# Performance work log

Hardware: AMD Instinct MI355X
Metric: run time of the kernel (lower is better)

Reference implementation:

```python
import jax, jax.numpy as jnp
import numpy as np

DELTA_VAR = 0.5
DELTA_DIST = 1.5
ALPHA, BETA, GAMMA = 1.0, 1.0, 0.001
EPS = 1e-8


def _safe_sqrt(x):
    # sqrt with zero (sub)gradient at 0, matching torch.norm's subgradient
    pos = x > 0
    return jnp.sqrt(jnp.where(pos, x, 1.0)) * pos


def setup_inputs() -> dict:
    key = jax.random.key(0)
    k1, k2, k3 = jax.random.split(key, 3)
    B, F, H, W, K = 8, 16, 384, 384, 24
    x = jax.random.normal(k1, (B, F, H, W), dtype=jnp.float32)
    n_clusters = jax.random.randint(k2, (B,), 2, K + 1).astype(jnp.int32)
    # per-pixel instance labels, in-range per sample
    labels = jax.random.randint(k3, (B, H * W), 0, K) % n_clusters[:, None]
    target = jax.nn.one_hot(labels, K, dtype=jnp.float32)  # (B, L, K)
    target = target.transpose(0, 2, 1).reshape(B, K, H, W)
    return {"input": x, "target": target, "n_clusters": n_clusters}


def reference(input, target, n_clusters):
    B, F, H, W = input.shape
    K = target.shape[1]
    x = input.reshape(B, F, H * W)          # (b, f, l)
    t = target.reshape(B, K, H * W)         # (b, c, l)
    nc = n_clusters.astype(x.dtype)         # (b,)
    valid = (jnp.arange(K)[None, :] < n_clusters[:, None]).astype(x.dtype)  # (b, c)

    # ---- cluster means (masked segment mean; padded clusters -> 0) ----
    t_sum = t.sum(-1)                                        # (b, c)
    sums = jnp.einsum('bfl,bcl->bfc', x, t)                  # (b, f, c)
    means = sums / (t_sum[:, None, :] + EPS) * valid[:, None, :]

    # ---- variance term: ||x_l - mu_c||_2 via quadratic expansion ----
    x2 = jnp.sum(x * x, axis=1)                              # (b, l)
    m2 = jnp.sum(means * means, axis=1)                      # (b, c)
    xm = jnp.einsum('bfl,bfc->bcl', x, means)                # (b, c, l)
    d2 = jnp.maximum(x2[:, None, :] - 2.0 * xm + m2[:, :, None], 0.0)
    dist = _safe_sqrt(d2)                                    # (b, c, l)
    var = jnp.maximum(dist - DELTA_VAR, 0.0) ** 2 * t        # (b, c, l)
    c_var = var.sum(-1) / (t_sum + EPS)                      # (b, c)
    var_per = (c_var * valid).sum(-1) / (nc + EPS)
    var_term = jnp.sum(var_per * (nc > 0)) / B

    # ---- distance term: hinge on pairwise mean distances ----
    mm = jnp.einsum('bfc,bfd->bcd', means, means)            # (b, c, c)
    pd2 = jnp.maximum(m2[:, :, None] - 2.0 * mm + m2[:, None, :], 0.0)
    pdist = _safe_sqrt(pd2)                                  # (b, c, c)
    offdiag = 1.0 - jnp.eye(K, dtype=x.dtype)
    pair_mask = valid[:, :, None] * valid[:, None, :] * offdiag
    hinge = jnp.maximum(2.0 * DELTA_DIST - pdist, 0.0) ** 2 * pair_mask
    dist_per = hinge.sum((1, 2)) / (2.0 * nc * (nc - 1.0) + EPS)
    dist_term = jnp.sum(dist_per * (nc > 1)) / B

    # ---- regularization term: mean over valid clusters of ||mu_c|| ----
    norms = _safe_sqrt(m2)                                   # (b, c)
    reg_term = jnp.sum((norms * valid).sum(-1) / nc) / B

    return ALPHA * var_term + BETA * dist_term + GAMMA * reg_term
```

## Files before the change

### kernel.cpp

```cpp
#include <hip/hip_runtime.h>

#define B 8
#define F 16
#define K 24
#define L 147456
#define CHUNK1 1024
#define NCH1 144
#define TOTCH 1152
#define EPSF 1e-8f
#define DELTA_VAR 0.5f
#define DELTA_DIST 1.5f
#define GAMMA 0.001f

typedef float fx4 __attribute__((ext_vector_type(4)));
typedef short bf16x8 __attribute__((ext_vector_type(8)));
typedef float f32x4 __attribute__((ext_vector_type(4)));

#define OFF_CNTP 1769472
#define OFF_VARP 1880064
#define OFF_CNT  1990656
#define OFF_MEAN 1991424
#define OFF_LAB  2003968

__device__ __forceinline__ short to_bf16(float v) {
    unsigned u = __float_as_uint(v);
    return (short)((u + 0x7FFFu + ((u >> 16) & 1u)) >> 16);
}

__global__ __launch_bounds__(256, 3) void k1_sums(
        const float* __restrict__ t, const float* __restrict__ x,
        unsigned char* __restrict__ labels, float* __restrict__ cnt_part,
        float* __restrict__ sum_part) {
    const int gblk = blockIdx.x;
    const int b = gblk / NCH1;
    const int ch = gblk % NCH1;
    const int tid = threadIdx.x;
    const int wave = tid >> 6;
    const int lane = tid & 63;
    const int n = lane & 15;
    const int q = lane >> 4;

    __shared__ unsigned char slab[CHUNK1];
    __shared__ float hist[4][32];
    __shared__ float sacc[4][F * K];

    if (lane < 32) hist[wave][lane] = 0.f;

    const float* xr = x + (size_t)(b * F + n) * L + ch * CHUNK1 + wave * 256 + q * 8;
    fx4 xv[16];
    #pragma unroll
    for (int it = 0; it < 8; ++it) {
        xv[2 * it]     = *(const fx4*)(xr + it * 32);
        xv[2 * it + 1] = *(const fx4*)(xr + it * 32 + 4);
    }
    __builtin_amdgcn_sched_barrier(0);

    const int px = ch * CHUNK1 + tid * 4;
    const fx4* t4 = (const fx4*)t;
    int lab0 = 0, lab1 = 0, lab2 = 0, lab3 = 0;
    #pragma unroll
    for (int h = 0; h < 3; ++h) {
        fx4 tv[8];
        #pragma unroll
        for (int j = 0; j < 8; ++j)
            tv[j] = __builtin_nontemporal_load(
                &t4[((size_t)(b * K + h * 8 + j) * L + px) >> 2]);
        __builtin_amdgcn_sched_barrier(0);
        #pragma unroll
        for (int j = 0; j < 8; ++j) {
            int c = h * 8 + j;
            lab0 += c * (tv[j].x > 0.5f);
            lab1 += c * (tv[j].y > 0.5f);
            lab2 += c * (tv[j].z > 0.5f);
            lab3 += c * (tv[j].w > 0.5f);
        }
    }
    uchar4 lv = make_uchar4((unsigned char)lab0, (unsigned char)lab1,
                            (unsigned char)lab2, (unsigned char)lab3);
    *(uchar4*)&labels[(size_t)b * L + px] = lv;
    *(uchar4*)&slab[tid * 4] = lv;
    atomicAdd(&hist[wave][lab0], 1.f);
    atomicAdd(&hist[wave][lab1], 1.f);
    atomicAdd(&hist[wave][lab2], 1.f);
    atomicAdd(&hist[wave][lab3], 1.f);
    __syncthreads();
    if (tid < K) {
        float v = hist[0][tid] + hist[1][tid] + hist[2][tid] + hist[3][tid];
        cnt_part[tid * TOTCH + gblk] = v;
    }

    const unsigned char* sl = slab + wave * 256 + q * 8;
    f32x4 acc0 = {0.f, 0.f, 0.f, 0.f};
    f32x4 acc1 = {0.f, 0.f, 0.f, 0.f};
    #pragma unroll
    for (int it = 0; it < 8; ++it) {
        unsigned l0 = *(const unsigned*)(sl + it * 32);
        unsigned l1 = *(const unsigned*)(sl + it * 32 + 4);
        fx4 xa = xv[2 * it], xc = xv[2 * it + 1];

        bf16x8 afrag;
        afrag[0] = to_bf16(xa.x); afrag[1] = to_bf16(xa.y);
        afrag[2] = to_bf16(xa.z); afrag[3] = to_bf16(xa.w);
        afrag[4] = to_bf16(xc.x); afrag[5] = to_bf16(xc.y);
        afrag[6] = to_bf16(xc.z); afrag[7] = to_bf16(xc.w);

        bf16x8 bf0, bf1;
        #pragma unroll
        for (int j = 0; j < 8; ++j) {
            int lj = (j < 4) ? ((l0 >> (8 * j)) & 0xFF) : ((l1 >> (8 * (j - 4))) & 0xFF);
            bf0[j] = (lj == n)      ? (short)0x3F80 : (short)0;
            bf1[j] = (lj == n + 16) ? (short)0x3F80 : (short)0;
        }
        acc0 = __builtin_amdgcn_mfma_f32_16x16x32_bf16(afrag, bf0, acc0, 0, 0, 0);
        acc1 = __builtin_amdgcn_mfma_f32_16x16x32_bf16(afrag, bf1, acc1, 0, 0, 0);
    }

    #pragma unroll
    for (int r = 0; r < 4; ++r) {
        int f = q * 4 + r;
        sacc[wave][f * K + n] = acc0[r];
        if (n < 8) sacc[wave][f * K + 16 + n] = acc1[r];
    }
    __syncthreads();
    for (int i = tid; i < F * K; i += 256) {
        float v = sacc[0][i] + sacc[1][i] + sacc[2][i] + sacc[3][i];
        sum_part[(size_t)i * TOTCH + gblk] = v;
    }
}

__global__ __launch_bounds__(256) void k2_means(const float* __restrict__ cnt_part,
                                                const float* __restrict__ sum_part,
                                                const int* __restrict__ ncl,
                                                float* __restrict__ counts,
                                                float* __restrict__ means) {
    const int idx = blockIdx.x * 4 + (threadIdx.x >> 6);
    const int lane = threadIdx.x & 63;
    const int b = idx / (F * K);
    const int r = idx % (F * K);
    const int c = r % K;

    const float* crow = cnt_part + c * TOTCH + b * NCH1;
    const float* srow = sum_part + (size_t)r * TOTCH + b * NCH1;
    float cv = crow[lane] + crow[lane + 64] + ((lane < 16) ? crow[lane + 128] : 0.f);
    float sv = srow[lane] + srow[lane + 64] + ((lane < 16) ? srow[lane + 128] : 0.f);
    #pragma unroll
    for (int off = 32; off > 0; off >>= 1) {
        cv += __shfl_down(cv, off);
        sv += __shfl_down(sv, off);
    }
    if (lane == 0) {
        if (r < K) counts[b * K + c] = cv;
        float valid = (c < ncl[b]) ? 1.f : 0.f;
        means[b * F * K + r] = sv / (cv + EPSF) * valid;
    }
}

__global__ __launch_bounds__(256, 4) void k3_var(
        const float* __restrict__ x, const unsigned char* __restrict__ labels,
        const float* __restrict__ means, float* __restrict__ var_part) {
    const int gblk = blockIdx.x;
    const int b = gblk / NCH1;
    const int ch = gblk % NCH1;
    const int tid = threadIdx.x;
    const int wave = tid >> 6;
    const int lane = tid & 63;

    __shared__ float m[F * K];
    __shared__ float hist[4][32];

    const int px = ch * CHUNK1 + tid * 4;
    uchar4 lv = *(const uchar4*)&labels[(size_t)b * L + px];
    const fx4* x4 = (const fx4*)x;
    fx4 xv[F];
    #pragma unroll
    for (int f = 0; f < F; ++f)
        xv[f] = x4[((size_t)(b * F + f) * L + px) >> 2];
    __builtin_amdgcn_sched_barrier(0);

    for (int i = tid; i < F * K; i += 256) m[i] = means[b * F * K + i];
    if (lane < 32) hist[wave][lane] = 0.f;
    __syncthreads();

    float d0 = 0.f, d1 = 0.f, d2 = 0.f, d3 = 0.f;
    #pragma unroll
    for (int f = 0; f < F; ++f) {
        float u0 = xv[f].x - m[f * K + lv.x]; d0 += u0 * u0;
        float u1 = xv[f].y - m[f * K + lv.y]; d1 += u1 * u1;
        float u2 = xv[f].z - m[f * K + lv.z]; d2 += u2 * u2;
        float u3 = xv[f].w - m[f * K + lv.w]; d3 += u3 * u3;
    }
    float s0 = fmaxf(sqrtf(d0) - DELTA_VAR, 0.f); s0 *= s0;
    float s1 = fmaxf(sqrtf(d1) - DELTA_VAR, 0.f); s1 *= s1;
    float s2 = fmaxf(sqrtf(d2) - DELTA_VAR, 0.f); s2 *= s2;
    float s3 = fmaxf(sqrtf(d3) - DELTA_VAR, 0.f); s3 *= s3;
    atomicAdd(&hist[wave][lv.x], s0);
    atomicAdd(&hist[wave][lv.y], s1);
    atomicAdd(&hist[wave][lv.z], s2);
    atomicAdd(&hist[wave][lv.w], s3);
    __syncthreads();
    if (tid < K) {
        float v = hist[0][tid] + hist[1][tid] + hist[2][tid] + hist[3][tid];
        var_part[tid * TOTCH + gblk] = v;
    }
}

__global__ __launch_bounds__(256) void k4_finish(
        const float* __restrict__ var_part, const float* __restrict__ means,
        const float* __restrict__ counts, const int* __restrict__ ncl,
        float* __restrict__ out) {
    __shared__ float big[B * F * K];
    __shared__ float vs[192], cn[192], red[256];
    const int tid = threadIdx.x;

    for (int i = tid; i < B * F * K; i += 256) big[i] = means[i];
    if (tid < 192) {
        int bb = tid / K, c = tid % K;
        const float* row = var_part + c * TOTCH + bb * NCH1;
        float s = 0.f;
        #pragma unroll 8
        for (int j = 0; j < NCH1; ++j) s += row[j];
        vs[tid] = s;
        cn[tid] = counts[tid];
    }
    __syncthreads();

    float total = 0.f;
    for (int idx = tid; idx < B * K * K; idx += 256) {
        int bb = idx / (K * K);
        int r = idx % (K * K);
        int c = r / K;
        int d = r % K;
        int ncb = ncl[bb];
        float fnc = (float)ncb;
        if (d == 0 && c < ncb && ncb > 0) {
            float cv = vs[bb * K + c] / (cn[bb * K + c] + EPSF);
            total += cv / (fnc + EPSF) * (1.0f / B);
            float m2 = 0.f;
            #pragma unroll
            for (int f = 0; f < F; ++f) {
                float mv = big[(bb * F + f) * K + c];
                m2 += mv * mv;
            }
            total += GAMMA * sqrtf(m2) / fnc * (1.0f / B);
        }
        if (c != d && c < ncb && d < ncb && ncb > 1) {
            float pd2 = 0.f;
            #pragma unroll
            for (int f = 0; f < F; ++f) {
                float diff = big[(bb * F + f) * K + c] - big[(bb * F + f) * K + d];
                pd2 += diff * diff;
            }
            float h = fmaxf(2.f * DELTA_DIST - sqrtf(pd2), 0.f);
            total += h * h / (2.f * fnc * (fnc - 1.f) + EPSF) * (1.0f / B);
        }
    }
    red[tid] = total;
    __syncthreads();
    for (int s = 128; s > 0; s >>= 1) {
        if (tid < s) red[tid] += red[tid + s];
        __syncthreads();
    }
    if (tid == 0) out[0] = red[0];
}

extern "C" void kernel_launch(void* const* d_in, const int* in_sizes, int n_in,
                              void* d_out, int out_size, void* d_ws, size_t ws_size,
                              hipStream_t stream) {
    const float* x = (const float*)d_in[0];
    const float* t = (const float*)d_in[1];
    const int* ncl = (const int*)d_in[2];
    float* out = (float*)d_out;

    char* ws = (char*)d_ws;
    float* sum_part = (float*)ws;
    float* cnt_part = (float*)(ws + OFF_CNTP);
    float* var_part = (float*)(ws + OFF_VARP);
    float* counts   = (float*)(ws + OFF_CNT);
    float* means    = (float*)(ws + OFF_MEAN);
    unsigned char* labels = (unsigned char*)(ws + OFF_LAB);

    k1_sums <<<TOTCH, 256, 0, stream>>>(t, x, labels, cnt_part, sum_part);
    k2_means<<<768, 256, 0, stream>>>(cnt_part, sum_part, ncl, counts, means);
    k3_var  <<<TOTCH, 256, 0, stream>>>(x, labels, means, var_part);
    k4_finish<<<1, 256, 0, stream>>>(var_part, means, counts, ncl, out);
}
```

Before: 243.6 us.

## Interleave batches across blocks, transpose sum partials, parallelize variance reduction

Blocks are remapped so consecutive block IDs cycle over batches instead of walking chunks within one batch. The k1 partial-sum layout becomes chunk-major so its writes are contiguous, and k2 reads are strided to match. The serial per-thread variance reduction in the single-block finish kernel moves into a new 48-block wave-shuffle reduction kernel. The extra launch adds a little overhead, and k2 now reads strided instead of contiguous.

```diff
diff --git a/kernel.cpp b/kernel.cpp
--- a/kernel.cpp
+++ b/kernel.cpp
@@ -19,8 +19,9 @@
 #define OFF_CNTP 1769472
 #define OFF_VARP 1880064
 #define OFF_CNT  1990656
-#define OFF_MEAN 1991424
-#define OFF_LAB  2003968
+#define OFF_VSUM 1991424
+#define OFF_MEAN 1992192
+#define OFF_LAB  2004480
 
 __device__ __forceinline__ short to_bf16(float v) {
     unsigned u = __float_as_uint(v);
@@ -31,9 +32,9 @@
         const float* __restrict__ t, const float* __restrict__ x,
         unsigned char* __restrict__ labels, float* __restrict__ cnt_part,
         float* __restrict__ sum_part) {
-    const int gblk = blockIdx.x;
-    const int b = gblk / NCH1;
-    const int ch = gblk % NCH1;
+    const int b = blockIdx.x & 7;
+    const int ch = blockIdx.x >> 3;
+    const int gblk = b * NCH1 + ch;
     const int tid = threadIdx.x;
     const int wave = tid >> 6;
     const int lane = tid & 63;
@@ -124,7 +125,7 @@
     __syncthreads();
     for (int i = tid; i < F * K; i += 256) {
         float v = sacc[0][i] + sacc[1][i] + sacc[2][i] + sacc[3][i];
-        sum_part[(size_t)i * TOTCH + gblk] = v;
+        sum_part[(size_t)gblk * (F * K) + i] = v;
     }
 }
 
@@ -140,9 +141,10 @@
     const int c = r % K;
 
     const float* crow = cnt_part + c * TOTCH + b * NCH1;
-    const float* srow = sum_part + (size_t)r * TOTCH + b * NCH1;
+    const float* srow = sum_part + (size_t)(b * NCH1) * (F * K) + r;
     float cv = crow[lane] + crow[lane + 64] + ((lane < 16) ? crow[lane + 128] : 0.f);
-    float sv = srow[lane] + srow[lane + 64] + ((lane < 16) ? srow[lane + 128] : 0.f);
+    float sv = srow[(size_t)lane * (F * K)] + srow[(size_t)(lane + 64) * (F * K)]
+             + ((lane < 16) ? srow[(size_t)(lane + 128) * (F * K)] : 0.f);
     #pragma unroll
     for (int off = 32; off > 0; off >>= 1) {
         cv += __shfl_down(cv, off);
@@ -158,9 +160,9 @@
 __global__ __launch_bounds__(256, 4) void k3_var(
         const float* __restrict__ x, const unsigned char* __restrict__ labels,
         const float* __restrict__ means, float* __restrict__ var_part) {
-    const int gblk = blockIdx.x;
-    const int b = gblk / NCH1;
-    const int ch = gblk % NCH1;
+    const int b = blockIdx.x & 7;
+    const int ch = blockIdx.x >> 3;
+    const int gblk = b * NCH1 + ch;
     const int tid = threadIdx.x;
     const int wave = tid >> 6;
     const int lane = tid & 63;
@@ -204,8 +206,21 @@
     }
 }
 
+__global__ __launch_bounds__(256) void k3r_reduce(const float* __restrict__ var_part,
+                                                  float* __restrict__ varsums) {
+    const int bc = blockIdx.x * 4 + (threadIdx.x >> 6);
+    const int lane = threadIdx.x & 63;
+    const int b = bc / K;
+    const int c = bc % K;
+    const float* row = var_part + c * TOTCH + b * NCH1;
+    float s = row[lane] + row[lane + 64] + ((lane < 16) ? row[lane + 128] : 0.f);
+    #pragma unroll
+    for (int off = 32; off > 0; off >>= 1) s += __shfl_down(s, off);
+    if (lane == 0) varsums[bc] = s;
+}
+
 __global__ __launch_bounds__(256) void k4_finish(
-        const float* __restrict__ var_part, const float* __restrict__ means,
+        const float* __restrict__ varsums, const float* __restrict__ means,
         const float* __restrict__ counts, const int* __restrict__ ncl,
         float* __restrict__ out) {
     __shared__ float big[B * F * K];
@@ -214,12 +229,7 @@
 
     for (int i = tid; i < B * F * K; i += 256) big[i] = means[i];
     if (tid < 192) {
-        int bb = tid / K, c = tid % K;
-        const float* row = var_part + c * TOTCH + bb * NCH1;
-        float s = 0.f;
-        #pragma unroll 8
-        for (int j = 0; j < NCH1; ++j) s += row[j];
-        vs[tid] = s;
+        vs[tid] = varsums[tid];
         cn[tid] = counts[tid];
     }
     __syncthreads();
@@ -276,11 +286,13 @@
     float* cnt_part = (float*)(ws + OFF_CNTP);
     float* var_part = (float*)(ws + OFF_VARP);
     float* counts   = (float*)(ws + OFF_CNT);
+    float* varsums  = (float*)(ws + OFF_VSUM);
     float* means    = (float*)(ws + OFF_MEAN);
     unsigned char* labels = (unsigned char*)(ws + OFF_LAB);
 
-    k1_sums <<<TOTCH, 256, 0, stream>>>(t, x, labels, cnt_part, sum_part);
-    k2_means<<<768, 256, 0, stream>>>(cnt_part, sum_part, ncl, counts, means);
-    k3_var  <<<TOTCH, 256, 0, stream>>>(x, labels, means, var_part);
-    k4_finish<<<1, 256, 0, stream>>>(var_part, means, counts, ncl, out);
-}
+    k1_sums   <<<TOTCH, 256, 0, stream>>>(t, x, labels, cnt_part, sum_part);
+    k2_means  <<<768, 256, 0, stream>>>(cnt_part, sum_part, ncl, counts, means);
+    k3_var    <<<TOTCH, 256, 0, stream>>>(x, labels, means, var_part);
+    k3r_reduce<<<48, 256, 0, stream>>>(var_part, varsums);
+    k4_finish <<<1, 256, 0, stream>>>(varsums, means, counts, ncl, out);
+}
```

Measured after the change: 241.3 us. About the same (-0.9%).
